# Kernel optimization log

Measured on AMD Instinct MI355X. Metric: run time of the kernel, lower is better.

## Reference

```python
import jax, jax.numpy as jnp
import numpy as np

N, E, L = 10000, 160000, 4
IN, HID, HEADS, OUT = 15, 128, 4, 5
C = HID              # per-head out_channels of TransformerConv
HC = HEADS * C       # concatenated width = 512
EPS = 1e-5


def _w(k, shape, fan_in):
    return (jax.random.normal(k, shape, jnp.float32) / np.sqrt(fan_in)).astype(jnp.float32)


def setup_inputs() -> dict:
    key = jax.random.key(0)
    ks = jax.random.split(key, 24)
    return {
        "x": jax.random.normal(ks[0], (N, IN), jnp.float32),
        "edge_index": jax.random.randint(ks[1], (2, E), 0, N, dtype=jnp.int32),
        # input / output projections
        "W_in": _w(ks[2], (IN, HID), IN), "b_in": jnp.zeros((HID,), jnp.float32),
        "W_out": _w(ks[3], (HID, OUT), HID), "b_out": jnp.zeros((OUT,), jnp.float32),
        # stacked per-layer TransformerConv params (L leading dim)
        "Wq": _w(ks[4], (L, HID, HC), HID), "bq": jnp.zeros((L, HC), jnp.float32),
        "Wk": _w(ks[5], (L, HID, HC), HID), "bk": jnp.zeros((L, HC), jnp.float32),
        "Wv": _w(ks[6], (L, HID, HC), HID), "bv": jnp.zeros((L, HC), jnp.float32),
        "Wskip": _w(ks[7], (L, HID, HC), HID), "bskip": jnp.zeros((L, HC), jnp.float32),
        "Wbeta": _w(ks[8], (L, 3 * HC, 1), 3 * HC),
        "ln_w": jnp.ones((L, HC), jnp.float32), "ln_b": jnp.zeros((L, HC), jnp.float32),
        "Wproj": _w(ks[9], (L, HC, HID), HC), "bproj": jnp.zeros((L, HID), jnp.float32),
    }


def _forward(x, edge_index, W_in, b_in, Wq, bq, Wk, bk, Wv, bv,
             Wskip, bskip, Wbeta, ln_w, ln_b, Wproj, bproj, W_out, b_out):
    src, dst = edge_index[0], edge_index[1]  # message j->i aggregated at dst
    h = x @ W_in + b_in  # [N, HID]

    def layer(h, p):
        Wq_, bq_, Wk_, bk_, Wv_, bv_, Ws_, bs_, Wb_, lw, lb, Wp_, bp_ = p
        q = (h @ Wq_ + bq_).reshape(N, HEADS, C)
        k = (h @ Wk_ + bk_).reshape(N, HEADS, C)
        v = (h @ Wv_ + bv_).reshape(N, HEADS, C)
        # attention logits per edge/head: [E, HEADS]
        logits = (q[dst] * k[src]).sum(-1) / jnp.sqrt(jnp.float32(C))
        # segment softmax over incoming edges of each target node
        m = jax.ops.segment_max(logits, dst, num_segments=N)
        ex = jnp.exp(logits - m[dst])
        den = jax.ops.segment_sum(ex, dst, num_segments=N)
        alpha = ex / (den[dst] + 1e-16)
        out = jax.ops.segment_sum(v[src] * alpha[..., None], dst,
                                  num_segments=N).reshape(N, HC)
        # beta-gated skip (TransformerConv beta=True)
        skip = h @ Ws_ + bs_
        beta = jax.nn.sigmoid(jnp.concatenate([out, skip, out - skip], -1) @ Wb_)  # [N,1]
        out = beta * skip + (1.0 - beta) * out
        # PyG LayerNorm, mode='graph' (single graph): normalize over all elements
        xc = out - out.mean()
        out = xc / (jnp.sqrt((xc * xc).mean()) + EPS) * lw + lb
        out = out @ Wp_ + bp_
        return jax.nn.relu(out + h), None

    params = (Wq, bq, Wk, bk, Wv, bv, Wskip, bskip, Wbeta, ln_w, ln_b, Wproj, bproj)
    h, _ = jax.lax.scan(layer, h, params)
    return h @ W_out + b_out


def reference(x, edge_index, W_in, b_in, Wq, bq, Wk, bk, Wv, bv,
              Wskip, bskip, Wbeta, ln_w, ln_b, Wproj, bproj, W_out, b_out):
    return _forward(x, edge_index, W_in, b_in, Wq, bq, Wk, bk, Wv, bv,
                    Wskip, bskip, Wbeta, ln_w, ln_b, Wproj, bproj, W_out, b_out)
```

## Files before the change

### kernel.cpp

```cpp
#include <hip/hip_runtime.h>
#include <math.h>

#define NN 10000
#define NE 160000
#define HCW 512
#define CH 128
#define NLAYERS 4
#define LN_EPS 1e-5f
#define NBUCK 128

typedef short bf16x8 __attribute__((ext_vector_type(8)));
typedef float f32x4 __attribute__((ext_vector_type(4)));

__device__ inline unsigned short f2bf(float f) {
    union { float f; unsigned int u; } x; x.f = f;
    unsigned int u = x.u;
    return (unsigned short)((u + 0x7FFFu + ((u >> 16) & 1u)) >> 16);
}
__device__ inline float bf2f(unsigned short s) {
    union { unsigned int u; float f; } x; x.u = ((unsigned int)s) << 16;
    return x.f;
}
__device__ inline float lo16(unsigned int u) {
    union { unsigned int x; float f; } v; v.x = u << 16; return v.f;
}
__device__ inline float hi16(unsigned int u) {
    union { unsigned int x; float f; } v; v.x = u & 0xffff0000u; return v.f;
}

template<int CTRL>
__device__ inline float dppadd(float x) {
    int y = __builtin_amdgcn_update_dpp(0, __float_as_int(x), CTRL, 0xF, 0xF, true);
    return x + __int_as_float(y);
}
__device__ inline float red16(float x) {
    x = dppadd<0x128>(x);
    x = dppadd<0x124>(x);
    x = dppadd<0x122>(x);
    x = dppadd<0x121>(x);
    return x;
}
__device__ inline float red64(float x) {
    x = red16(x);
    x += __shfl_xor(x, 16, 64);
    x += __shfl_xor(x, 32, 64);
    return x;
}

__device__ inline float dot8(const float4& q0, const float4& q1, const uint4& kk) {
    return q0.x * lo16(kk.x) + q0.y * hi16(kk.x)
         + q0.z * lo16(kk.y) + q0.w * hi16(kk.y)
         + q1.x * lo16(kk.z) + q1.y * hi16(kk.z)
         + q1.z * lo16(kk.w) + q1.w * hi16(kk.w);
}

__global__ void k_init(int* cnt, int* fill, float* stats) {
    int i = blockIdx.x * blockDim.x + threadIdx.x;
    if (i < NN) { cnt[i] = 0; fill[i] = 0; }
    if (i < NLAYERS * NBUCK * 16) stats[i] = 0.f;
}

__global__ void k_count(const int* __restrict__ dst, int* __restrict__ cnt) {
    int e = blockIdx.x * blockDim.x + threadIdx.x;
    if (e < NE) atomicAdd(&cnt[dst[e]], 1);
}

__global__ __launch_bounds__(1024) void k_scan(const int* __restrict__ cnt, int* __restrict__ offs) {
    __shared__ int sh[1024];
    __shared__ int carry;
    if (threadIdx.x == 0) carry = 0;
    __syncthreads();
    for (int base = 0; base < NN; base += 1024) {
        int i = base + threadIdx.x;
        int v = (i < NN) ? cnt[i] : 0;
        sh[threadIdx.x] = v;
        __syncthreads();
        for (int off = 1; off < 1024; off <<= 1) {
            int t = (threadIdx.x >= off) ? sh[threadIdx.x - off] : 0;
            __syncthreads();
            sh[threadIdx.x] += t;
            __syncthreads();
        }
        int incl = sh[threadIdx.x];
        if (i < NN) offs[i] = carry + incl - v;
        __syncthreads();
        if (threadIdx.x == 1023) carry += sh[1023];
        __syncthreads();
    }
    if (threadIdx.x == 0) offs[NN] = carry;
}

__global__ void k_fill(const int* __restrict__ src, const int* __restrict__ dst,
                       const int* __restrict__ offs, int* __restrict__ fill,
                       int* __restrict__ col) {
    int e = blockIdx.x * blockDim.x + threadIdx.x;
    if (e < NE) {
        int d = dst[e];
        int p = offs[d] + atomicAdd(&fill[d], 1);
        col[p] = src[e];
    }
}

__global__ void k_wconv(const float* __restrict__ Wq, const float* __restrict__ Wk,
                        const float* __restrict__ Wv, const float* __restrict__ Ws,
                        const float* __restrict__ Wp,
                        unsigned short* __restrict__ wt_qkvs,
                        unsigned short* __restrict__ wpt) {
    int id = blockIdx.x * blockDim.x + threadIdx.x;
    if (id < NLAYERS * 2048 * 128) {
        int l = id >> 18;
        int rem = id & 262143;
        int n = rem >> 7, k = rem & 127;
        int mat = n >> 9, wcol = n & 511;
        const float* W = (mat == 0) ? Wq : (mat == 1) ? Wk : (mat == 2) ? Wv : Ws;
        wt_qkvs[id] = f2bf(W[(size_t)l * 65536 + k * 512 + wcol]);
    } else if (id < NLAYERS * 2048 * 128 + NLAYERS * 128 * 512) {
        int id2 = id - NLAYERS * 2048 * 128;
        int l = id2 >> 16;
        int rem = id2 & 65535;
        int n = rem >> 9, k = rem & 511;
        wpt[(size_t)l * 65536 + n * 512 + k] = f2bf(Wp[(size_t)l * 65536 + k * 128 + n]);
    }
}

__global__ __launch_bounds__(128) void k_inproj(const float* __restrict__ x,
                                                const float* __restrict__ W,
                                                const float* __restrict__ b,
                                                float* __restrict__ h,
                                                unsigned short* __restrict__ h_bf) {
    int n = blockIdx.x;
    int j = threadIdx.x;
    float acc = b[j];
#pragma unroll
    for (int i = 0; i < 15; i++) acc += x[n * 15 + i] * W[i * 128 + j];
    h[n * 128 + j] = acc;
    h_bf[n * 128 + j] = f2bf(acc);
}

__global__ __launch_bounds__(256) void k_qkvs_mfma(
    const unsigned short* __restrict__ h_bf,
    const unsigned short* __restrict__ Wt,
    const float* __restrict__ bq, const float* __restrict__ bk,
    const float* __restrict__ bv, const float* __restrict__ bs,
    float* __restrict__ qb, unsigned short* __restrict__ kv16,
    float* __restrict__ sb) {
    __shared__ unsigned short As[128 * 128];
    __shared__ unsigned short Bs[128 * 128];
    int row0 = blockIdx.x * 128;
    int n0 = blockIdx.y * 128;
    int t = threadIdx.x;
#pragma unroll
    for (int i = 0; i < 8; i++) {
        int c = t + i * 256;
        int r = c >> 4, cc = c & 15;
        int gr = row0 + r;
        uint4 v = make_uint4(0, 0, 0, 0);
        if (gr < NN) v = *(const uint4*)(h_bf + (size_t)gr * 128 + cc * 8);
        int sc = (r << 4) | (cc ^ (r & 7));
        *(uint4*)(As + sc * 8) = v;
    }
#pragma unroll
    for (int i = 0; i < 8; i++) {
        int c = t + i * 256;
        int r = c >> 4, cc = c & 15;
        uint4 v = *(const uint4*)(Wt + (size_t)(n0 + r) * 128 + cc * 8);
        int sc = (r << 4) | (cc ^ (r & 7));
        *(uint4*)(Bs + sc * 8) = v;
    }
    __syncthreads();
    int wave = t >> 6, lane = t & 63;
    int wr = (wave >> 1) * 64, wc = (wave & 1) * 64;
    int lr = lane & 15, lk = lane >> 4;
    f32x4 acc[4][4] = {};
#pragma unroll
    for (int ks = 0; ks < 4; ks++) {
        bf16x8 a[4], b[4];
#pragma unroll
        for (int mi = 0; mi < 4; mi++) {
            int r = wr + mi * 16 + lr;
            int cc = (ks * 4 + lk) ^ (r & 7);
            a[mi] = *(const bf16x8*)(As + (((r << 4) | cc) * 8));
        }
#pragma unroll
        for (int ni = 0; ni < 4; ni++) {
            int r = wc + ni * 16 + lr;
            int cc = (ks * 4 + lk) ^ (r & 7);
            b[ni] = *(const bf16x8*)(Bs + (((r << 4) | cc) * 8));
        }
#pragma unroll
        for (int mi = 0; mi < 4; mi++)
#pragma unroll
            for (int ni = 0; ni < 4; ni++)
                acc[mi][ni] = __builtin_amdgcn_mfma_f32_16x16x32_bf16(a[mi], b[ni], acc[mi][ni], 0, 0, 0);
    }
#pragma unroll
    for (int ni = 0; ni < 4; ni++) {
        int gc = n0 + wc + ni * 16 + lr;
        int mat = gc >> 9, wcol = gc & 511;
        float bias = ((mat == 0) ? bq : (mat == 1) ? bk : (mat == 2) ? bv : bs)[wcol];
#pragma unroll
        for (int mi = 0; mi < 4; mi++) {
            int gr0 = row0 + wr + mi * 16 + 4 * lk;
#pragma unroll
            for (int r = 0; r < 4; r++) {
                int grr = gr0 + r;
                if (grr < NN) {
                    float val = acc[mi][ni][r] + bias;
                    if (mat == 0)      qb[(size_t)grr * 512 + wcol] = val;
                    else if (mat == 3) sb[(size_t)grr * 512 + wcol] = val;
                    else if (mat == 1) kv16[((size_t)grr << 10) + wcol] = f2bf(val);
                    else               kv16[((size_t)grr << 10) + 512 + wcol] = f2bf(val);
                }
            }
        }
    }
}

__global__ __launch_bounds__(256) void k_attn_beta(
    const float* __restrict__ qb,
    const unsigned short* __restrict__ kv16,
    const float* __restrict__ skip,
    const float* __restrict__ Wb,
    const int* __restrict__ offs, const int* __restrict__ col,
    float* __restrict__ gated, float* __restrict__ stats) {
    int n = blockIdx.x;
    int head = threadIdx.x >> 6;
    int lane = threadIdx.x & 63;
    int g = lane >> 4;
    int subl = lane & 15;
    const int hbase = head * CH;
    const int off = hbase + subl * 8;
    const float* qrow = qb + (size_t)n * HCW + off;
    const float4 q0 = *(const float4*)qrow;
    const float4 q1 = *(const float4*)(qrow + 4);
    int beg = offs[n], end = offs[n + 1];
    const float scale = 0.08838834764831845f;

    float mA = -INFINITY, sA = 0.f, mB = -INFINITY, sB = 0.f;
    float4 a0A = {0.f, 0.f, 0.f, 0.f}, a1A = {0.f, 0.f, 0.f, 0.f};
    float4 a0B = {0.f, 0.f, 0.f, 0.f}, a1B = {0.f, 0.f, 0.f, 0.f};

    for (int p = beg + g; p < end; p += 8) {
        int pB = p + 4;
        bool hasB = (pB < end);
        int snA = col[p];
        int snB = hasB ? col[pB] : snA;
        const unsigned short* bA = kv16 + ((size_t)snA << 10) + off;
        const unsigned short* bB = kv16 + ((size_t)snB << 10) + off;
        uint4 kkA = *(const uint4*)bA;
        uint4 vvA = *(const uint4*)(bA + 512);
        uint4 kkB = *(const uint4*)bB;
        uint4 vvB = *(const uint4*)(bB + 512);
        float dA = dot8(q0, q1, kkA);
        float dB = dot8(q0, q1, kkB);
        dA = red16(dA);
        dB = red16(dB);
        float lA = dA * scale;
        float lB = dB * scale;
        if (lA <= mA + 8.f) {
            float w = __expf(lA - mA);
            sA += w;
            a0A.x += w * lo16(vvA.x); a0A.y += w * hi16(vvA.x);
            a0A.z += w * lo16(vvA.y); a0A.w += w * hi16(vvA.y);
            a1A.x += w * lo16(vvA.z); a1A.y += w * hi16(vvA.z);
            a1A.z += w * lo16(vvA.w); a1A.w += w * hi16(vvA.w);
        } else {
            float sc = __expf(mA - lA);
            sA = sA * sc + 1.f;
            a0A.x = a0A.x * sc + lo16(vvA.x); a0A.y = a0A.y * sc + hi16(vvA.x);
            a0A.z = a0A.z * sc + lo16(vvA.y); a0A.w = a0A.w * sc + hi16(vvA.y);
            a1A.x = a1A.x * sc + lo16(vvA.z); a1A.y = a1A.y * sc + hi16(vvA.z);
            a1A.z = a1A.z * sc + lo16(vvA.w); a1A.w = a1A.w * sc + hi16(vvA.w);
            mA = lA;
        }
        if (hasB) {
            if (lB <= mB + 8.f) {
                float w = __expf(lB - mB);
                sB += w;
                a0B.x += w * lo16(vvB.x); a0B.y += w * hi16(vvB.x);
                a0B.z += w * lo16(vvB.y); a0B.w += w * hi16(vvB.y);
                a1B.x += w * lo16(vvB.z); a1B.y += w * hi16(vvB.z);
                a1B.z += w * lo16(vvB.w); a1B.w += w * hi16(vvB.w);
            } else {
                float sc = __expf(mB - lB);
                sB = sB * sc + 1.f;
                a0B.x = a0B.x * sc + lo16(vvB.x); a0B.y = a0B.y * sc + hi16(vvB.x);
                a0B.z = a0B.z * sc + lo16(vvB.y); a0B.w = a0B.w * sc + hi16(vvB.y);
                a1B.x = a1B.x * sc + lo16(vvB.z); a1B.y = a1B.y * sc + hi16(vvB.z);
                a1B.z = a1B.z * sc + lo16(vvB.w); a1B.w = a1B.w * sc + hi16(vvB.w);
                mB = lB;
            }
        }
    }
    {
        float mn = fmaxf(mA, mB);
        float c1 = (sA > 0.f) ? __expf(mA - mn) : 0.f;
        float c2 = (sB > 0.f) ? __expf(mB - mn) : 0.f;
        sA = sA * c1 + sB * c2;
        a0A.x = a0A.x * c1 + a0B.x * c2; a0A.y = a0A.y * c1 + a0B.y * c2;
        a0A.z = a0A.z * c1 + a0B.z * c2; a0A.w = a0A.w * c1 + a0B.w * c2;
        a1A.x = a1A.x * c1 + a1B.x * c2; a1A.y = a1A.y * c1 + a1B.y * c2;
        a1A.z = a1A.z * c1 + a1B.z * c2; a1A.w = a1A.w * c1 + a1B.w * c2;
        mA = mn;
    }
#pragma unroll
    for (int off2 = 16; off2 <= 32; off2 <<= 1) {
        float m_o = __shfl_xor(mA, off2, 64);
        float s_o = __shfl_xor(sA, off2, 64);
        float4 b0, b1;
        b0.x = __shfl_xor(a0A.x, off2, 64); b0.y = __shfl_xor(a0A.y, off2, 64);
        b0.z = __shfl_xor(a0A.z, off2, 64); b0.w = __shfl_xor(a0A.w, off2, 64);
        b1.x = __shfl_xor(a1A.x, off2, 64); b1.y = __shfl_xor(a1A.y, off2, 64);
        b1.z = __shfl_xor(a1A.z, off2, 64); b1.w = __shfl_xor(a1A.w, off2, 64);
        float mn = fmaxf(mA, m_o);
        float c1 = (sA > 0.f) ? __expf(mA - mn) : 0.f;
        float c2 = (s_o > 0.f) ? __expf(m_o - mn) : 0.f;
        sA = sA * c1 + s_o * c2;
        a0A.x = a0A.x * c1 + b0.x * c2; a0A.y = a0A.y * c1 + b0.y * c2;
        a0A.z = a0A.z * c1 + b0.z * c2; a0A.w = a0A.w * c1 + b0.w * c2;
        a1A.x = a1A.x * c1 + b1.x * c2; a1A.y = a1A.y * c1 + b1.y * c2;
        a1A.z = a1A.z * c1 + b1.z * c2; a1A.w = a1A.w * c1 + b1.w * c2;
        mA = mn;
    }
    float inv = (sA > 0.f) ? 1.f / sA : 0.f;

    __shared__ float att_s[512];
    if (g == 0) {
        float4 o0 = {a0A.x * inv, a0A.y * inv, a0A.z * inv, a0A.w * inv};
        float4 o1 = {a1A.x * inv, a1A.y * inv, a1A.z * inv, a1A.w * inv};
        *(float4*)(att_s + off) = o0;
        *(float4*)(att_s + off + 4) = o1;
    }
    __syncthreads();

    int c0 = hbase + lane * 2;
    float o0 = att_s[c0], o1 = att_s[c0 + 1];
    float2 sk = ((const float2*)(skip + (size_t)n * HCW + hbase))[lane];
    float part = o0 * Wb[c0] + o1 * Wb[c0 + 1]
               + sk.x * Wb[512 + c0] + sk.y * Wb[512 + c0 + 1]
               + (o0 - sk.x) * Wb[1024 + c0] + (o1 - sk.y) * Wb[1024 + c0 + 1];
    part = red64(part);
    __shared__ float red[4];
    if (lane == 0) red[head] = part;
    __syncthreads();
    float tot = red[0] + red[1] + red[2] + red[3];
    float beta = 1.f / (1.f + __expf(-tot));
    float gx = beta * sk.x + (1.f - beta) * o0;
    float gy = beta * sk.y + (1.f - beta) * o1;
    ((float2*)(gated + (size_t)n * HCW + hbase))[lane] = make_float2(gx, gy);

    float ls = red64(gx + gy);
    float lq = red64(gx * gx + gy * gy);
    __shared__ float r2[8];
    if (lane == 0) { r2[head] = ls; r2[4 + head] = lq; }
    __syncthreads();
    if (threadIdx.x == 0) {
        int b = n & (NBUCK - 1);
        atomicAdd(&stats[b * 16], r2[0] + r2[1] + r2[2] + r2[3]);
        atomicAdd(&stats[b * 16 + 1], r2[4] + r2[5] + r2[6] + r2[7]);
    }
}

__global__ __launch_bounds__(512) void k_proj_mfma(
    const float* __restrict__ gated,
    const unsigned short* __restrict__ Wpt,
    const float* __restrict__ bp,
    const float* __restrict__ lw, const float* __restrict__ lb,
    const float* __restrict__ stats,
    float* __restrict__ h, unsigned short* __restrict__ h_bf) {
    __shared__ unsigned short As[64 * 128];
    __shared__ unsigned short Bs[128 * 128];
    int row0 = blockIdx.x * 64;
    int t = threadIdx.x;
    float ssum = 0.f, sq = 0.f;
#pragma unroll 16
    for (int i = 0; i < NBUCK; i++) { ssum += stats[i * 16]; sq += stats[i * 16 + 1]; }
    const float invM = 1.f / (NN * 512.f);
    float mean = ssum * invM;
    float ms = sq * invM - mean * mean;
    float rstd = 1.f / (sqrtf(fmaxf(ms, 0.f)) + LN_EPS);
    int wave = t >> 6, lane = t & 63;
    int wr = (wave >> 1) * 16, wc = (wave & 1) * 64;
    int lr = lane & 15, lk = lane >> 4;
    f32x4 acc[4] = {};
    for (int kc = 0; kc < 4; kc++) {
        __syncthreads();
#pragma unroll
        for (int i = 0; i < 2; i++) {
            int c = t + i * 512;
            int r = c >> 4, cc = c & 15;
            int gr = row0 + r;
            int gk = kc * 128 + cc * 8;
            unsigned short u[8];
            if (gr < NN) {
                const float* gp = gated + (size_t)gr * 512 + gk;
#pragma unroll
                for (int j = 0; j < 8; j++) {
                    float v = (gp[j] - mean) * rstd * lw[gk + j] + lb[gk + j];
                    u[j] = f2bf(v);
                }
            } else {
#pragma unroll
                for (int j = 0; j < 8; j++) u[j] = 0;
            }
            int sc = (r << 4) | (cc ^ (r & 7));
            *(uint4*)(As + sc * 8) = *(uint4*)u;
        }
#pragma unroll
        for (int i = 0; i < 4; i++) {
            int c = t + i * 512;
            int r = c >> 4, cc = c & 15;
            uint4 v = *(const uint4*)(Wpt + (size_t)r * 512 + kc * 128 + cc * 8);
            int sc = (r << 4) | (cc ^ (r & 7));
            *(uint4*)(Bs + sc * 8) = v;
        }
        __syncthreads();
#pragma unroll
        for (int ks = 0; ks < 4; ks++) {
            bf16x8 a, b[4];
            {
                int r = wr + lr;
                int cc = (ks * 4 + lk) ^ (r & 7);
                a = *(const bf16x8*)(As + (((r << 4) | cc) * 8));
            }
#pragma unroll
            for (int ni = 0; ni < 4; ni++) {
                int r = wc + ni * 16 + lr;
                int cc = (ks * 4 + lk) ^ (r & 7);
                b[ni] = *(const bf16x8*)(Bs + (((r << 4) | cc) * 8));
            }
#pragma unroll
            for (int ni = 0; ni < 4; ni++)
                acc[ni] = __builtin_amdgcn_mfma_f32_16x16x32_bf16(a, b[ni], acc[ni], 0, 0, 0);
        }
    }
#pragma unroll
    for (int ni = 0; ni < 4; ni++) {
        int gc = wc + ni * 16 + lr;
        float bias = bp[gc];
        int gr0 = row0 + wr + 4 * lk;
#pragma unroll
        for (int r = 0; r < 4; r++) {
            int grr = gr0 + r;
            if (grr < NN) {
                float o = acc[ni][r] + bias + h[(size_t)grr * 128 + gc];
                o = fmaxf(o, 0.f);
                h[(size_t)grr * 128 + gc] = o;
                h_bf[(size_t)grr * 128 + gc] = f2bf(o);
            }
        }
    }
}

__global__ void k_out(const float* __restrict__ h, const float* __restrict__ W,
                      const float* __restrict__ b, float* __restrict__ out) {
    int i = blockIdx.x * blockDim.x + threadIdx.x;
    if (i >= NN * 5) return;
    int n = i / 5, j = i % 5;
    float acc = b[j];
    for (int k = 0; k < 128; k++) acc += h[(size_t)n * 128 + k] * W[k * 5 + j];
    out[i] = acc;
}

extern "C" void kernel_launch(void* const* d_in, const int* in_sizes, int n_in,
                              void* d_out, int out_size, void* d_ws, size_t ws_size,
                              hipStream_t stream) {
    const float* x     = (const float*)d_in[0];
    const int* ei      = (const int*)d_in[1];
    const float* W_in  = (const float*)d_in[2];
    const float* b_in  = (const float*)d_in[3];
    const float* W_out = (const float*)d_in[4];
    const float* b_out = (const float*)d_in[5];
    const float* Wq    = (const float*)d_in[6];
    const float* bq    = (const float*)d_in[7];
    const float* Wk    = (const float*)d_in[8];
    const float* bk    = (const float*)d_in[9];
    const float* Wv    = (const float*)d_in[10];
    const float* bv    = (const float*)d_in[11];
    const float* Wsk   = (const float*)d_in[12];
    const float* bsk   = (const float*)d_in[13];
    const float* Wbeta = (const float*)d_in[14];
    const float* ln_w  = (const float*)d_in[15];
    const float* ln_b  = (const float*)d_in[16];
    const float* Wproj = (const float*)d_in[17];
    const float* bproj = (const float*)d_in[18];
    float* out = (float*)d_out;

    float* h     = (float*)d_ws;
    float* qb    = h + (size_t)NN * 128;
    float* sb    = qb + (size_t)NN * 512;
    float* stats = sb + (size_t)NN * 512;
    int* offs = (int*)(stats + NLAYERS * NBUCK * 16);
    int* cnt  = offs + (NN + 1);
    int* fill = cnt + NN;
    int* col  = fill + NN;
    unsigned short* h_bf = (unsigned short*)(((uintptr_t)(col + NE) + 15) & ~(uintptr_t)15);
    unsigned short* kv16 = h_bf + (size_t)NN * 128;
    unsigned short* wt_qkvs = kv16 + (size_t)NN * 1024;
    unsigned short* wpt = wt_qkvs + (size_t)NLAYERS * 2048 * 128;
    float* gated = qb;

    const int* src = ei;
    const int* dst = ei + NE;

    k_init<<<(NN + 255) / 256, 256, 0, stream>>>(cnt, fill, stats);
    k_count<<<(NE + 255) / 256, 256, 0, stream>>>(dst, cnt);
    k_scan<<<1, 1024, 0, stream>>>(cnt, offs);
    k_fill<<<(NE + 255) / 256, 256, 0, stream>>>(src, dst, offs, fill, col);
    {
        int tot = NLAYERS * 2048 * 128 + NLAYERS * 128 * 512;
        k_wconv<<<(tot + 255) / 256, 256, 0, stream>>>(Wq, Wk, Wv, Wsk, Wproj, wt_qkvs, wpt);
    }
    k_inproj<<<NN, 128, 0, stream>>>(x, W_in, b_in, h, h_bf);

    for (int l = 0; l < NLAYERS; ++l) {
        const unsigned short* Wt_ = wt_qkvs + (size_t)l * 2048 * 128;
        const unsigned short* Wp_ = wpt + (size_t)l * 128 * 512;
        const float* bq_ = bq + l * 512;
        const float* bk_ = bk + l * 512;
        const float* bv_ = bv + l * 512;
        const float* bs_ = bsk + l * 512;
        const float* Wb_ = Wbeta + (size_t)l * 1536;
        const float* lw_ = ln_w + l * 512;
        const float* lb_ = ln_b + l * 512;
        const float* bp_ = bproj + l * 128;
        float* st = stats + (size_t)l * NBUCK * 16;

        dim3 g1((NN + 127) / 128, 16);
        k_qkvs_mfma<<<g1, 256, 0, stream>>>(h_bf, Wt_, bq_, bk_, bv_, bs_,
                                            qb, kv16, sb);
        k_attn_beta<<<NN, 256, 0, stream>>>(qb, kv16, sb, Wb_, offs, col, gated, st);
        k_proj_mfma<<<(NN + 63) / 64, 512, 0, stream>>>(gated, Wp_, bp_, lw_, lb_, st, h, h_bf);
    }
    k_out<<<(NN * 5 + 255) / 256, 256, 0, stream>>>(h, W_out, b_out, out);
}
```

Before: 556.1 us.

## Store q, skip and gated activations in bf16 and reuse A tile across two N-subtiles

Query, skip and gated intermediates move from fp32 to bf16 storage, which halves their global write and read traffic across the QKVS GEMM, the attention kernel and the projection kernel. The QKVS GEMM now has each block handle two 128-column subtiles and keep the A fragments in registers, so half as many blocks reload the h tile. LayerNorm statistics are computed from the rounded bf16 gated values to stay consistent with what the projection reads. The cost is extra rounding error on q, skip and gated, plus higher register pressure from the 16 held A fragments.

```diff
diff --git a/kernel.cpp b/kernel.cpp
--- a/kernel.cpp
+++ b/kernel.cpp
@@ -142,12 +142,11 @@
     const unsigned short* __restrict__ Wt,
     const float* __restrict__ bq, const float* __restrict__ bk,
     const float* __restrict__ bv, const float* __restrict__ bs,
-    float* __restrict__ qb, unsigned short* __restrict__ kv16,
-    float* __restrict__ sb) {
+    unsigned short* __restrict__ qb16, unsigned short* __restrict__ kv16,
+    unsigned short* __restrict__ sb16) {
     __shared__ unsigned short As[128 * 128];
     __shared__ unsigned short Bs[128 * 128];
     int row0 = blockIdx.x * 128;
-    int n0 = blockIdx.y * 128;
     int t = threadIdx.x;
 #pragma unroll
     for (int i = 0; i < 8; i++) {
@@ -159,57 +158,66 @@
         int sc = (r << 4) | (cc ^ (r & 7));
         *(uint4*)(As + sc * 8) = v;
     }
-#pragma unroll
-    for (int i = 0; i < 8; i++) {
-        int c = t + i * 256;
-        int r = c >> 4, cc = c & 15;
-        uint4 v = *(const uint4*)(Wt + (size_t)(n0 + r) * 128 + cc * 8);
-        int sc = (r << 4) | (cc ^ (r & 7));
-        *(uint4*)(Bs + sc * 8) = v;
-    }
-    __syncthreads();
     int wave = t >> 6, lane = t & 63;
     int wr = (wave >> 1) * 64, wc = (wave & 1) * 64;
     int lr = lane & 15, lk = lane >> 4;
-    f32x4 acc[4][4] = {};
-#pragma unroll
-    for (int ks = 0; ks < 4; ks++) {
-        bf16x8 a[4], b[4];
-#pragma unroll
-        for (int mi = 0; mi < 4; mi++) {
-            int r = wr + mi * 16 + lr;
-            int cc = (ks * 4 + lk) ^ (r & 7);
-            a[mi] = *(const bf16x8*)(As + (((r << 4) | cc) * 8));
+    bf16x8 afr[16];
+    for (int sub = 0; sub < 2; sub++) {
+        int n0 = blockIdx.y * 256 + sub * 128;
+        __syncthreads();
+#pragma unroll
+        for (int i = 0; i < 8; i++) {
+            int c = t + i * 256;
+            int r = c >> 4, cc = c & 15;
+            uint4 v = *(const uint4*)(Wt + (size_t)(n0 + r) * 128 + cc * 8);
+            int sc = (r << 4) | (cc ^ (r & 7));
+            *(uint4*)(Bs + sc * 8) = v;
+        }
+        if (sub == 0) {
+#pragma unroll
+            for (int ks = 0; ks < 4; ks++)
+#pragma unroll
+                for (int mi = 0; mi < 4; mi++) {
+                    int r = wr + mi * 16 + lr;
+                    int cc = (ks * 4 + lk) ^ (r & 7);
+                    afr[ks * 4 + mi] = *(const bf16x8*)(As + (((r << 4) | cc) * 8));
+                }
+        }
+        __syncthreads();
+        f32x4 acc[4][4] = {};
+#pragma unroll
+        for (int ks = 0; ks < 4; ks++) {
+            bf16x8 b[4];
+#pragma unroll
+            for (int ni = 0; ni < 4; ni++) {
+                int r = wc + ni * 16 + lr;
+                int cc = (ks * 4 + lk) ^ (r & 7);
+                b[ni] = *(const bf16x8*)(Bs + (((r << 4) | cc) * 8));
+            }
+#pragma unroll
+            for (int mi = 0; mi < 4; mi++)
+#pragma unroll
+                for (int ni = 0; ni < 4; ni++)
+                    acc[mi][ni] = __builtin_amdgcn_mfma_f32_16x16x32_bf16(afr[ks * 4 + mi], b[ni], acc[mi][ni], 0, 0, 0);
         }
 #pragma unroll
         for (int ni = 0; ni < 4; ni++) {
-            int r = wc + ni * 16 + lr;
-            int cc = (ks * 4 + lk) ^ (r & 7);
-            b[ni] = *(const bf16x8*)(Bs + (((r << 4) | cc) * 8));
-        }
-#pragma unroll
-        for (int mi = 0; mi < 4; mi++)
-#pragma unroll
-            for (int ni = 0; ni < 4; ni++)
-                acc[mi][ni] = __builtin_amdgcn_mfma_f32_16x16x32_bf16(a[mi], b[ni], acc[mi][ni], 0, 0, 0);
-    }
-#pragma unroll
-    for (int ni = 0; ni < 4; ni++) {
-        int gc = n0 + wc + ni * 16 + lr;
-        int mat = gc >> 9, wcol = gc & 511;
-        float bias = ((mat == 0) ? bq : (mat == 1) ? bk : (mat == 2) ? bv : bs)[wcol];
-#pragma unroll
-        for (int mi = 0; mi < 4; mi++) {
-            int gr0 = row0 + wr + mi * 16 + 4 * lk;
-#pragma unroll
-            for (int r = 0; r < 4; r++) {
-                int grr = gr0 + r;
-                if (grr < NN) {
-                    float val = acc[mi][ni][r] + bias;
-                    if (mat == 0)      qb[(size_t)grr * 512 + wcol] = val;
-                    else if (mat == 3) sb[(size_t)grr * 512 + wcol] = val;
-                    else if (mat == 1) kv16[((size_t)grr << 10) + wcol] = f2bf(val);
-                    else               kv16[((size_t)grr << 10) + 512 + wcol] = f2bf(val);
+            int gc = n0 + wc + ni * 16 + lr;
+            int mat = gc >> 9, wcol = gc & 511;
+            float bias = ((mat == 0) ? bq : (mat == 1) ? bk : (mat == 2) ? bv : bs)[wcol];
+#pragma unroll
+            for (int mi = 0; mi < 4; mi++) {
+                int gr0 = row0 + wr + mi * 16 + 4 * lk;
+#pragma unroll
+                for (int r = 0; r < 4; r++) {
+                    int grr = gr0 + r;
+                    if (grr < NN) {
+                        unsigned short val = f2bf(acc[mi][ni][r] + bias);
+                        if (mat == 0)      qb16[(size_t)grr * 512 + wcol] = val;
+                        else if (mat == 1) kv16[((size_t)grr << 10) + wcol] = val;
+                        else if (mat == 2) kv16[((size_t)grr << 10) + 512 + wcol] = val;
+                        else               sb16[(size_t)grr * 512 + wcol] = val;
+                    }
                 }
             }
         }
@@ -217,12 +225,12 @@
 }
 
 __global__ __launch_bounds__(256) void k_attn_beta(
-    const float* __restrict__ qb,
+    const unsigned short* __restrict__ qb16,
     const unsigned short* __restrict__ kv16,
-    const float* __restrict__ skip,
+    const unsigned short* __restrict__ sb16,
     const float* __restrict__ Wb,
     const int* __restrict__ offs, const int* __restrict__ col,
-    float* __restrict__ gated, float* __restrict__ stats) {
+    unsigned short* __restrict__ gated16, float* __restrict__ stats) {
     int n = blockIdx.x;
     int head = threadIdx.x >> 6;
     int lane = threadIdx.x & 63;
@@ -230,9 +238,9 @@
     int subl = lane & 15;
     const int hbase = head * CH;
     const int off = hbase + subl * 8;
-    const float* qrow = qb + (size_t)n * HCW + off;
-    const float4 q0 = *(const float4*)qrow;
-    const float4 q1 = *(const float4*)(qrow + 4);
+    uint4 qq = *(const uint4*)(qb16 + (size_t)n * HCW + off);
+    float4 q0 = {lo16(qq.x), hi16(qq.x), lo16(qq.y), hi16(qq.y)};
+    float4 q1 = {lo16(qq.z), hi16(qq.z), lo16(qq.w), hi16(qq.w)};
     int beg = offs[n], end = offs[n + 1];
     const float scale = 0.08838834764831845f;
 
@@ -335,22 +343,25 @@
 
     int c0 = hbase + lane * 2;
     float o0 = att_s[c0], o1 = att_s[c0 + 1];
-    float2 sk = ((const float2*)(skip + (size_t)n * HCW + hbase))[lane];
+    unsigned int sku = *(const unsigned int*)(sb16 + (size_t)n * HCW + c0);
+    float skx = lo16(sku), sky = hi16(sku);
     float part = o0 * Wb[c0] + o1 * Wb[c0 + 1]
-               + sk.x * Wb[512 + c0] + sk.y * Wb[512 + c0 + 1]
-               + (o0 - sk.x) * Wb[1024 + c0] + (o1 - sk.y) * Wb[1024 + c0 + 1];
+               + skx * Wb[512 + c0] + sky * Wb[512 + c0 + 1]
+               + (o0 - skx) * Wb[1024 + c0] + (o1 - sky) * Wb[1024 + c0 + 1];
     part = red64(part);
     __shared__ float red[4];
     if (lane == 0) red[head] = part;
     __syncthreads();
     float tot = red[0] + red[1] + red[2] + red[3];
     float beta = 1.f / (1.f + __expf(-tot));
-    float gx = beta * sk.x + (1.f - beta) * o0;
-    float gy = beta * sk.y + (1.f - beta) * o1;
-    ((float2*)(gated + (size_t)n * HCW + hbase))[lane] = make_float2(gx, gy);
-
-    float ls = red64(gx + gy);
-    float lq = red64(gx * gx + gy * gy);
+    float gx = beta * skx + (1.f - beta) * o0;
+    float gy = beta * sky + (1.f - beta) * o1;
+    unsigned int gu = (unsigned int)f2bf(gx) | ((unsigned int)f2bf(gy) << 16);
+    *(unsigned int*)(gated16 + (size_t)n * HCW + c0) = gu;
+
+    float gxr = lo16(gu), gyr = hi16(gu);
+    float ls = red64(gxr + gyr);
+    float lq = red64(gxr * gxr + gyr * gyr);
     __shared__ float r2[8];
     if (lane == 0) { r2[head] = ls; r2[4 + head] = lq; }
     __syncthreads();
@@ -362,7 +373,7 @@
 }
 
 __global__ __launch_bounds__(512) void k_proj_mfma(
-    const float* __restrict__ gated,
+    const unsigned short* __restrict__ gated16,
     const unsigned short* __restrict__ Wpt,
     const float* __restrict__ bp,
     const float* __restrict__ lw, const float* __restrict__ lb,
@@ -393,12 +404,12 @@
             int gk = kc * 128 + cc * 8;
             unsigned short u[8];
             if (gr < NN) {
-                const float* gp = gated + (size_t)gr * 512 + gk;
-#pragma unroll
-                for (int j = 0; j < 8; j++) {
-                    float v = (gp[j] - mean) * rstd * lw[gk + j] + lb[gk + j];
-                    u[j] = f2bf(v);
-                }
+                uint4 gv = *(const uint4*)(gated16 + (size_t)gr * 512 + gk);
+                float vals[8] = {lo16(gv.x), hi16(gv.x), lo16(gv.y), hi16(gv.y),
+                                 lo16(gv.z), hi16(gv.z), lo16(gv.w), hi16(gv.w)};
+#pragma unroll
+                for (int j = 0; j < 8; j++)
+                    u[j] = f2bf((vals[j] - mean) * rstd * lw[gk + j] + lb[gk + j]);
             } else {
 #pragma unroll
                 for (int j = 0; j < 8; j++) u[j] = 0;
@@ -487,18 +498,18 @@
     float* out = (float*)d_out;
 
     float* h     = (float*)d_ws;
-    float* qb    = h + (size_t)NN * 128;
-    float* sb    = qb + (size_t)NN * 512;
-    float* stats = sb + (size_t)NN * 512;
+    float* stats = h + (size_t)NN * 128;
     int* offs = (int*)(stats + NLAYERS * NBUCK * 16);
     int* cnt  = offs + (NN + 1);
     int* fill = cnt + NN;
     int* col  = fill + NN;
     unsigned short* h_bf = (unsigned short*)(((uintptr_t)(col + NE) + 15) & ~(uintptr_t)15);
-    unsigned short* kv16 = h_bf + (size_t)NN * 128;
+    unsigned short* qb16 = h_bf + (size_t)NN * 128;
+    unsigned short* sb16 = qb16 + (size_t)NN * 512;
+    unsigned short* kv16 = sb16 + (size_t)NN * 512;
     unsigned short* wt_qkvs = kv16 + (size_t)NN * 1024;
     unsigned short* wpt = wt_qkvs + (size_t)NLAYERS * 2048 * 128;
-    float* gated = qb;
+    unsigned short* gated16 = qb16;
 
     const int* src = ei;
     const int* dst = ei + NE;
@@ -526,11 +537,11 @@
         const float* bp_ = bproj + l * 128;
         float* st = stats + (size_t)l * NBUCK * 16;
 
-        dim3 g1((NN + 127) / 128, 16);
+        dim3 g1((NN + 127) / 128, 8);
         k_qkvs_mfma<<<g1, 256, 0, stream>>>(h_bf, Wt_, bq_, bk_, bv_, bs_,
-                                            qb, kv16, sb);
-        k_attn_beta<<<NN, 256, 0, stream>>>(qb, kv16, sb, Wb_, offs, col, gated, st);
-        k_proj_mfma<<<(NN + 63) / 64, 512, 0, stream>>>(gated, Wp_, bp_, lw_, lb_, st, h, h_bf);
+                                            qb16, kv16, sb16);
+        k_attn_beta<<<NN, 256, 0, stream>>>(qb16, kv16, sb16, Wb_, offs, col, gated16, st);
+        k_proj_mfma<<<(NN + 63) / 64, 512, 0, stream>>>(gated16, Wp_, bp_, lw_, lb_, st, h, h_bf);
     }
     k_out<<<(NN * 5 + 255) / 256, 256, 0, stream>>>(h, W_out, b_out, out);
 }
```

After: 678.7 us. 1.22x slower.
